# Kernel optimization log

Measured on AMD Instinct MI355X. Metric: run time of the kernel, lower is better.

The kernel has to match this reference:

```python
import jax, jax.numpy as jnp
import numpy as np

B, N, C, H, P, DP = 2, 1024, 768, 12, 4, 64
CH = C // H
SCALE = CH ** -0.5
EPS = 1e-5


def setup_inputs() -> dict:
    key = jax.random.key(0)
    ks = jax.random.split(key, 24)
    w = lambda k, s: jax.random.normal(k, s, jnp.float32) * 0.02
    inp = {
        'single': jax.random.normal(ks[0], (B, N, C), jnp.float32),
        'pair': jax.random.normal(ks[1], (B, N, N, DP), jnp.float32),
        'rot': jax.random.normal(ks[2], (B, N, 3, 3), jnp.float32),
        'trans': jax.random.normal(ks[3], (B, N, 3), jnp.float32),
        'mask': jnp.ones((B, N), dtype=bool),
        'Wq': w(ks[4], (C, C)), 'bq': jnp.zeros((C,), jnp.float32),
        'Wk': w(ks[5], (C, C)), 'bk': jnp.zeros((C,), jnp.float32),
        'Wv': w(ks[6], (C, C)), 'bv': jnp.zeros((C,), jnp.float32),
        'Wpb': w(ks[7], (DP, H)), 'bpb': jnp.zeros((H,), jnp.float32),
        'Wqp': w(ks[8], (C, H * P * 3)), 'bqp': jnp.zeros((H * P * 3,), jnp.float32),
        'Wkp': w(ks[9], (C, H * P * 3)), 'bkp': jnp.zeros((H * P * 3,), jnp.float32),
        'Wvp': w(ks[10], (C, H * P * 3)), 'bvp': jnp.zeros((H * P * 3,), jnp.float32),
        'Wo': w(ks[11], (C, C)), 'bo': jnp.zeros((C,), jnp.float32),
        'Wpo': w(ks[12], (H * P * 3, C)), 'bpo': jnp.zeros((C,), jnp.float32),
        'gamma': jnp.ones((C,), jnp.float32), 'beta': jnp.zeros((C,), jnp.float32),
    }
    return inp


def _ipa(single, pair, rot, trans, mask,
         Wq, bq, Wk, bk, Wv, bv, Wpb, bpb,
         Wqp, bqp, Wkp, bkp, Wvp, bvp,
         Wo, bo, Wpo, bpo, gamma, beta):
    # scalar q/k/v: [B,N,H,CH]
    q = (single @ Wq + bq).reshape(B, N, H, CH)
    k = (single @ Wk + bk).reshape(B, N, H, CH)
    v = (single @ Wv + bv).reshape(B, N, H, CH)
    # pair bias: [B,H,N,N]
    pair_bias = jnp.transpose(pair @ Wpb + bpb, (0, 3, 1, 2))
    # point q/k/v in local frames: [B,N,H,P,3]
    q_pts = (single @ Wqp + bqp).reshape(B, N, H, P, 3)
    k_pts = (single @ Wkp + bkp).reshape(B, N, H, P, 3)
    v_pts = (single @ Wvp + bvp).reshape(B, N, H, P, 3)
    # rotate into global frame and translate
    t = trans[:, :, None, None, :]  # [B,N,1,1,3]
    rt = lambda pts: jnp.einsum('bnhpd,bnde->bnhpe', pts, rot) + t
    q_pts, k_pts, v_pts = rt(q_pts), rt(k_pts), rt(v_pts)
    # squared norms: [B,H,N]
    q2 = jnp.transpose((q_pts ** 2).sum((3, 4)), (0, 2, 1))
    k2 = jnp.transpose((k_pts ** 2).sum((3, 4)), (0, 2, 1))
    # logits [B,H,M,N]
    scalar_logits = jnp.einsum('bmhc,bnhc->bhmn', q, k) * SCALE
    qk_pts = jnp.einsum('bmhpd,bnhpd->bhmn', q_pts, k_pts)
    point_logits = -0.5 * (q2[:, :, :, None] + k2[:, :, None, :] - 2.0 * qk_pts) * SCALE
    logits = scalar_logits + point_logits + pair_bias
    mask2d = mask[:, None, :, None] & mask[:, None, None, :]
    logits = jnp.where(mask2d, logits, -1e9)
    attn = jax.nn.softmax(logits, axis=-1)
    # dual output aggregation
    out_scalar = jnp.einsum('bhmn,bnhc->bmhc', attn, v).reshape(B, N, C)
    out_points = jnp.einsum('bhmn,bnhpd->bmhpd', attn, v_pts).reshape(B, N, H * P * 3)
    out = (out_scalar @ Wo + bo) + (out_points @ Wpo + bpo)
    x = single + out
    mu = x.mean(-1, keepdims=True)
    var = ((x - mu) ** 2).mean(-1, keepdims=True)
    return (x - mu) * jax.lax.rsqrt(var + EPS) * gamma + beta


def reference(single, pair, rot, trans, mask,
              Wq, bq, Wk, bk, Wv, bv, Wpb, bpb,
              Wqp, bqp, Wkp, bkp, Wvp, bvp,
              Wo, bo, Wpo, bpo, gamma, beta):
    return _ipa(single, pair, rot, trans, mask,
                Wq, bq, Wk, bk, Wv, bv, Wpb, bpb,
                Wqp, bqp, Wkp, bkp, Wvp, bvp,
                Wo, bo, Wpo, bpo, gamma, beta)
```

## Files before the change

### kernel.cpp

```cpp
#include <hip/hip_runtime.h>
#include <hip/hip_bf16.h>

#define B_ 2
#define N_ 1024
#define C_ 768
#define H_ 12
#define CH_ 64
#define P_ 4
#define DP_ 64
#define HP3 144
#define SCALE_ 0.125f
#define FATS 2816
#define K2_ 960
#define NCHUNK 2

typedef __attribute__((ext_vector_type(8))) short short8;
typedef __attribute__((ext_vector_type(4))) float f32x4;

__device__ __forceinline__ short f2bf(float f) {
  __hip_bfloat16 h = __float2bfloat16(f);
  return *reinterpret_cast<short*>(&h);
}
__device__ __forceinline__ float bf2f(unsigned short u) {
  __hip_bfloat16 h;
  *reinterpret_cast<unsigned short*>(&h) = u;
  return __bfloat162float(h);
}

__global__ __launch_bounds__(256) void prep_misc(
    const float* __restrict__ single, unsigned short* __restrict__ Sbf,
    const float* __restrict__ Wq, const float* __restrict__ Wk,
    const float* __restrict__ Wv, const float* __restrict__ Wqp,
    const float* __restrict__ Wkp, const float* __restrict__ Wvp,
    unsigned short* __restrict__ WT1,
    const float* __restrict__ Wo, const float* __restrict__ Wpo,
    unsigned short* __restrict__ W2T,
    const float* __restrict__ bq, const float* __restrict__ bk,
    const float* __restrict__ bv, const float* __restrict__ bqp,
    const float* __restrict__ bkp, const float* __restrict__ bvp,
    const float* __restrict__ bo, const float* __restrict__ bpo,
    float* __restrict__ bcat1, float* __restrict__ bias2)
{
  __shared__ float t[16][17];
  const int tid = threadIdx.x;
  const int bid = blockIdx.x;
  if (bid < 8448) {
    const int bx = bid % 48, by = bid / 48;
    const int rr = tid >> 4, cc = tid & 15;
    const int kk0 = bx * 16, nn0 = by * 16;
    const float* W = nullptr; int ncol0 = 0, Nw = 768;
    if (nn0 < 2304) {
      int s = nn0 / 768;
      W = (s == 0) ? Wq : (s == 1 ? Wk : Wv);
      ncol0 = nn0 - s * 768; Nw = 768;
    } else if (nn0 < 2736) {
      int s = (nn0 - 2304) / 144;
      W = (s == 0) ? Wqp : (s == 1 ? Wkp : Wvp);
      ncol0 = nn0 - 2304 - s * 144; Nw = 144;
    }
    t[rr][cc] = W ? W[(size_t)(kk0 + rr) * Nw + ncol0 + cc] : 0.f;
    __syncthreads();
    WT1[(size_t)(nn0 + rr) * 768 + kk0 + cc] = (unsigned short)f2bf(t[cc][rr]);
  } else if (bid < 11328) {
    const int lb = bid - 8448;
    const int bx = lb % 60, by = lb / 60;
    const int rr = tid >> 4, cc = tid & 15;
    const int kk0 = bx * 16, nn0 = by * 16;
    const int k2 = kk0 + rr, h = k2 / 80, c80 = k2 - h * 80;
    float v = 0.f;
    if (c80 < 64)      v = Wo[(size_t)(h * 64 + c80) * 768 + nn0 + cc];
    else if (c80 < 76) v = Wpo[(size_t)(h * 12 + c80 - 64) * 768 + nn0 + cc];
    t[rr][cc] = v;
    __syncthreads();
    W2T[(size_t)(nn0 + rr) * 960 + kk0 + cc] = (unsigned short)f2bf(t[cc][rr]);
  } else if (bid < 11339) {
    const int idx = (bid - 11328) * 256 + tid;
    if (idx < 2816) {
      float v = 0.f;
      if (idx < 2304) { int s = idx / 768; const float* p = s == 0 ? bq : (s == 1 ? bk : bv); v = p[idx - s * 768]; }
      else if (idx < 2736) { int s = (idx - 2304) / 144; const float* p = s == 0 ? bqp : (s == 1 ? bkp : bvp); v = p[idx - 2304 - s * 144]; }
      bcat1[idx] = v;
    }
    if (idx < 768) bias2[idx] = bo[idx] + bpo[idx];
  } else {
    const int idx = (bid - 11339) * 256 + tid;
    const float4 v = reinterpret_cast<const float4*>(single)[idx];
    union { unsigned short u[4]; uint2 v2; } o;
    o.u[0] = (unsigned short)f2bf(v.x); o.u[1] = (unsigned short)f2bf(v.y);
    o.u[2] = (unsigned short)f2bf(v.z); o.u[3] = (unsigned short)f2bf(v.w);
    reinterpret_cast<uint2*>(Sbf)[idx] = o.v2;
  }
}

template<int BM>
__global__ __launch_bounds__(256) void gemm_bf16(
    const unsigned short* __restrict__ A, int lda,
    const unsigned short* __restrict__ BT, int ldb, int K,
    float* __restrict__ out, int ldo, const float* __restrict__ bias)
{
  constexpr int BN = 64;
  constexpr int MI = BM / 32;
  constexpr int NJ = 2;
  __shared__ __align__(16) unsigned short As[BM][40];
  __shared__ __align__(16) unsigned short Bs[BN][40];
  const int tid = threadIdx.x;
  const int w = tid >> 6, l = tid & 63, r16 = l & 15, g = l >> 4;
  const int wr = w >> 1, wc = w & 1;
  const int bm = blockIdx.y * BM, bn = blockIdx.x * BN;
  f32x4 acc[MI][NJ];
  #pragma unroll
  for (int mi = 0; mi < MI; ++mi)
    #pragma unroll
    for (int nj = 0; nj < NJ; ++nj) {
      acc[mi][nj][0] = 0.f; acc[mi][nj][1] = 0.f;
      acc[mi][nj][2] = 0.f; acc[mi][nj][3] = 0.f;
    }
  for (int k0 = 0; k0 < K; k0 += 32) {
    #pragma unroll
    for (int i = 0; i < BM / 64; ++i) {
      const int idx = tid + 256 * i;
      const int row = idx >> 2, q4 = idx & 3;
      *(uint4*)&As[row][q4 * 8] =
          *(const uint4*)&A[(size_t)(bm + row) * lda + k0 + q4 * 8];
    }
    {
      const int row = tid >> 2, q4 = tid & 3;
      if (row < BN)
        *(uint4*)&Bs[row][q4 * 8] =
            *(const uint4*)&BT[(size_t)(bn + row) * ldb + k0 + q4 * 8];
    }
    __syncthreads();
    short8 af[MI], bfr[NJ];
    #pragma unroll
    for (int mi = 0; mi < MI; ++mi)
      af[mi] = *(const short8*)&As[wr * (BM / 2) + mi * 16 + r16][g * 8];
    #pragma unroll
    for (int nj = 0; nj < NJ; ++nj)
      bfr[nj] = *(const short8*)&Bs[wc * 32 + nj * 16 + r16][g * 8];
    #pragma unroll
    for (int mi = 0; mi < MI; ++mi)
      #pragma unroll
      for (int nj = 0; nj < NJ; ++nj)
        acc[mi][nj] = __builtin_amdgcn_mfma_f32_16x16x32_bf16(
            af[mi], bfr[nj], acc[mi][nj], 0, 0, 0);
    __syncthreads();
  }
  #pragma unroll
  for (int mi = 0; mi < MI; ++mi)
    #pragma unroll
    for (int nj = 0; nj < NJ; ++nj) {
      const int n = bn + wc * 32 + nj * 16 + r16;
      const float bn_ = bias[n];
      #pragma unroll
      for (int reg = 0; reg < 4; ++reg) {
        const int m = bm + wr * (BM / 2) + mi * 16 + g * 4 + reg;
        out[(size_t)m * ldo + n] = acc[mi][nj][reg] + bn_;
      }
    }
}

__global__ __launch_bounds__(128) void prep_qkv(
    const float* __restrict__ fat, const float* __restrict__ rot,
    const float* __restrict__ trans,
    __hip_bfloat16* __restrict__ Qaug, __hip_bfloat16* __restrict__ Kaug,
    __hip_bfloat16* __restrict__ Vtg)
{
  __shared__ float pts[3][12];
  __shared__ float s2[2];
  const int tid = threadIdx.x;
  const int bn = blockIdx.x, h = blockIdx.y;
  const int b = bn >> 10, n = bn & 1023;
  const int bh = b * H_ + h;
  const float* row = fat + (size_t)bn * FATS;
  if (tid < 36) {
    const int set = tid / 12, j = tid - set * 12;
    const int p = j / 3, e = j - p * 3;
    const float* src = row + 2304 + set * 144 + h * 12 + p * 3;
    const float d0 = src[0], d1 = src[1], d2 = src[2];
    const float* rr = rot + (size_t)bn * 9;
    pts[set][j] = d0 * rr[e] + d1 * rr[3 + e] + d2 * rr[6 + e]
                  + trans[(size_t)bn * 3 + e];
  }
  __syncthreads();
  if (tid < 2) {
    float s = 0.f;
    #pragma unroll
    for (int j = 0; j < 12; ++j) s += pts[tid][j] * pts[tid][j];
    s2[tid] = s;
  }
  __syncthreads();
  const int c = tid;
  if (c < 96) {
    float qv, kv;
    if (c < 64) {
      qv = SCALE_ * row[h * CH_ + c];
      kv = row[768 + h * CH_ + c];
    } else if (c < 76) {
      qv = SCALE_ * pts[0][c - 64];
      kv = pts[1][c - 64];
    } else if (c == 76) {
      qv = -0.5f * SCALE_ * s2[0];
      kv = 1.0f;
    } else if (c == 77) {
      qv = -0.5f * SCALE_;
      kv = s2[1];
    } else { qv = 0.f; kv = 0.f; }
    const size_t orow = ((size_t)bh << 10) + n;
    Qaug[orow * 96 + c] = __float2bfloat16(qv);
    Kaug[orow * 96 + c] = __float2bfloat16(kv);
  }
  if (c < 80) {
    float vv = 0.f;
    if (c < 64) vv = row[1536 + h * CH_ + c];
    else if (c < 76) vv = pts[2][c - 64];
    Vtg[(((size_t)bh * 80 + c) << 10) + n] = __float2bfloat16(vv);
  }
}

__global__ __launch_bounds__(256) void pair_bias_mfma(
    const float* __restrict__ pair, const float* __restrict__ Wpb,
    const float* __restrict__ bpb, unsigned short* __restrict__ pb)
{
  __shared__ __align__(16) short WpbT[16][72];
  __shared__ float bpb_s[16];
  __shared__ unsigned short PBs[256][18];
  const int tid = threadIdx.x;
  const int w = tid >> 6, l = tid & 63, r16 = l & 15, g = l >> 4;
  const size_t F0 = (size_t)blockIdx.x * 256;
  const int b = (int)(F0 >> 20);
  const int mn0 = (int)(F0 & 1048575);
  #pragma unroll
  for (int i = 0; i < 4; ++i) {
    int idx = tid + 256 * i;
    int hh = idx & 15, d = idx >> 4;
    WpbT[hh][d] = f2bf(hh < 12 ? Wpb[d * 12 + hh] : 0.f);
  }
  if (tid < 16) bpb_s[tid] = (tid < 12) ? bpb[tid] : 0.f;
  __syncthreads();
  #pragma unroll
  for (int rg = 0; rg < 4; ++rg) {
    const size_t Fr = F0 + w * 64 + rg * 16 + r16;
    const float* src = pair + Fr * 64;
    const float bias = bpb_s[r16];
    f32x4 acc;
    acc[0] = bias; acc[1] = bias; acc[2] = bias; acc[3] = bias;
    #pragma unroll
    for (int ks = 0; ks < 2; ++ks) {
      const f32x4 a0 = __builtin_nontemporal_load(
          reinterpret_cast<const f32x4*>(src + ks * 32 + g * 8));
      const f32x4 a1 = __builtin_nontemporal_load(
          reinterpret_cast<const f32x4*>(src + ks * 32 + g * 8 + 4));
      short8 ap;
      ap[0] = f2bf(a0[0]); ap[1] = f2bf(a0[1]); ap[2] = f2bf(a0[2]); ap[3] = f2bf(a0[3]);
      ap[4] = f2bf(a1[0]); ap[5] = f2bf(a1[1]); ap[6] = f2bf(a1[2]); ap[7] = f2bf(a1[3]);
      const short8 bw = *(const short8*)&WpbT[r16][ks * 32 + g * 8];
      acc = __builtin_amdgcn_mfma_f32_16x16x32_bf16(ap, bw, acc, 0, 0, 0);
    }
    #pragma unroll
    for (int reg = 0; reg < 4; ++reg)
      PBs[w * 64 + rg * 16 + 4 * g + reg][r16] = (unsigned short)f2bf(acc[reg]);
  }
  __syncthreads();
  #pragma unroll
  for (int hh = 0; hh < 12; ++hh)
    pb[((size_t)(b * 12 + hh) << 20) + mn0 + tid] = PBs[tid][hh];
}

__global__ __launch_bounds__(256) void flash_attn_part(
    const __hip_bfloat16* __restrict__ Qaug, const __hip_bfloat16* __restrict__ Kaug,
    const __hip_bfloat16* __restrict__ Vtg, const unsigned short* __restrict__ pb,
    unsigned short* __restrict__ pacc, float* __restrict__ pml)
{
  __shared__ __align__(16) short Ks[64][104];
  __shared__ __align__(16) short Vt[80][72];
  __shared__ __align__(16) short Ps[64][72];
  const int tid = threadIdx.x;
  const int w = tid >> 6, l = tid & 63, r16 = l & 15, g = l >> 4;
  const int m0 = blockIdx.x * 64;
  const int h = blockIdx.y;
  const int b = blockIdx.z >> 1, chunk = blockIdx.z & 1;
  const int bh = b * H_ + h;
  const uint4* Kg = (const uint4*)Kaug;
  const uint4* Vg = (const uint4*)Vtg;
  short8 qreg[3];
  {
    const unsigned short* qrow =
        (const unsigned short*)Qaug + (size_t)((bh << 10) + m0 + w * 16 + r16) * 96;
    #pragma unroll
    for (int ks = 0; ks < 3; ++ks)
      qreg[ks] = *(const short8*)&qrow[ks * 32 + g * 8];
  }
  float rm[4], rl[4];
  f32x4 acc[5];
  #pragma unroll
  for (int r = 0; r < 4; ++r) { rm[r] = -1e30f; rl[r] = 0.f; }
  #pragma unroll
  for (int ct = 0; ct < 5; ++ct) {
    acc[ct][0] = 0.f; acc[ct][1] = 0.f; acc[ct][2] = 0.f; acc[ct][3] = 0.f;
  }
  for (int t = chunk * (16 / NCHUNK); t < (chunk + 1) * (16 / NCHUNK); ++t) {
    const int n0 = t * 64;
    {
      const int r = tid >> 2, q = tid & 3;
      #pragma unroll
      for (int i = 0; i < 3; ++i) {
        const int c8 = q + 4 * i;
        *(uint4*)&Ks[r][c8 * 8] = Kg[(size_t)((bh << 10) + n0 + r) * 12 + c8];
      }
      #pragma unroll
      for (int i = 0; i < 3; ++i) {
        const int ch = tid + 256 * i;
        if (ch < 640) {
          const int cc = ch >> 3, j8 = ch & 7;
          *(uint4*)&Vt[cc][j8 * 8] = Vg[(size_t)(bh * 80 + cc) * 128 + (n0 >> 3) + j8];
        }
      }
    }
    f32x4 s[4];
    {
      const unsigned short* pbrow = pb + ((size_t)bh << 20) + n0 + r16;
      #pragma unroll
      for (int j = 0; j < 4; ++j)
        #pragma unroll
        for (int reg = 0; reg < 4; ++reg)
          s[j][reg] = bf2f(pbrow[((size_t)(m0 + w * 16 + 4 * g + reg) << 10) + 16 * j]);
    }
    __syncthreads();
    #pragma unroll
    for (int ks = 0; ks < 3; ++ks) {
      #pragma unroll
      for (int j = 0; j < 4; ++j) {
        const short8 bK = *(const short8*)&Ks[16 * j + r16][ks * 32 + g * 8];
        s[j] = __builtin_amdgcn_mfma_f32_16x16x32_bf16(qreg[ks], bK, s[j], 0, 0, 0);
      }
    }
    #pragma unroll
    for (int reg = 0; reg < 4; ++reg) {
      float tm = fmaxf(fmaxf(s[0][reg], s[1][reg]), fmaxf(s[2][reg], s[3][reg]));
      tm = fmaxf(tm, __shfl_xor(tm, 1));
      tm = fmaxf(tm, __shfl_xor(tm, 2));
      tm = fmaxf(tm, __shfl_xor(tm, 4));
      tm = fmaxf(tm, __shfl_xor(tm, 8));
      const float nm = fmaxf(rm[reg], tm);
      const float fac = __expf(rm[reg] - nm);
      rm[reg] = nm;
      float ps = 0.f;
      #pragma unroll
      for (int j = 0; j < 4; ++j) {
        const float p = __expf(s[j][reg] - nm);
        s[j][reg] = p;
        ps += p;
      }
      ps += __shfl_xor(ps, 1);
      ps += __shfl_xor(ps, 2);
      ps += __shfl_xor(ps, 4);
      ps += __shfl_xor(ps, 8);
      rl[reg] = rl[reg] * fac + ps;
      #pragma unroll
      for (int ct = 0; ct < 5; ++ct) acc[ct][reg] *= fac;
    }
    #pragma unroll
    for (int j = 0; j < 4; ++j)
      #pragma unroll
      for (int reg = 0; reg < 4; ++reg)
        Ps[w * 16 + 4 * g + reg][16 * j + r16] = f2bf(s[j][reg]);
    __syncthreads();
    #pragma unroll
    for (int ks = 0; ks < 2; ++ks) {
      const short8 aP = *(const short8*)&Ps[w * 16 + r16][ks * 32 + g * 8];
      #pragma unroll
      for (int ct = 0; ct < 5; ++ct) {
        const short8 bV = *(const short8*)&Vt[ct * 16 + r16][ks * 32 + g * 8];
        acc[ct] = __builtin_amdgcn_mfma_f32_16x16x32_bf16(aP, bV, acc[ct], 0, 0, 0);
      }
    }
    __syncthreads();
  }
  #pragma unroll
  for (int reg = 0; reg < 4; ++reg) {
    const int row = (bh << 10) + m0 + w * 16 + 4 * g + reg;
    const size_t base = ((size_t)chunk * 24576 + row) * 80;
    #pragma unroll
    for (int ct = 0; ct < 5; ++ct)
      pacc[base + ct * 16 + r16] = (unsigned short)f2bf(acc[ct][reg]);
    if (r16 == 0) {
      pml[((size_t)chunk * 24576 + row) * 2]     = rm[reg];
      pml[((size_t)chunk * 24576 + row) * 2 + 1] = rl[reg];
    }
  }
}

__global__ __launch_bounds__(256) void gemm2_fused(
    const unsigned short* __restrict__ pacc, const float* __restrict__ pml,
    const unsigned short* __restrict__ BT, float* __restrict__ out,
    const float* __restrict__ bias)
{
  __shared__ __align__(16) unsigned short As[64][40];
  __shared__ __align__(16) unsigned short Bs[64][40];
  __shared__ float w0_s[64][12], w1_s[64][12];
  const int tid = threadIdx.x;
  const int w = tid >> 6, l = tid & 63, r16 = l & 15, g = l >> 4;
  const int wr = w >> 1, wc = w & 1;
  const int bm = blockIdx.y * 64, bn = blockIdx.x * 64;
  for (int i = tid; i < 64 * 12; i += 256) {
    const int row = i / 12, h = i - row * 12;
    const int grow = bm + row;
    const int b = grow >> 10, m = grow & 1023;
    const size_t pr = ((size_t)(b * 12 + h) << 10) + m;
    const float m0 = pml[pr * 2],              l0 = pml[pr * 2 + 1];
    const float m1 = pml[(24576 + pr) * 2],    l1 = pml[(24576 + pr) * 2 + 1];
    const float M = fmaxf(m0, m1);
    const float e0 = __expf(m0 - M), e1 = __expf(m1 - M);
    const float inv = 1.f / (l0 * e0 + l1 * e1);
    w0_s[row][h] = e0 * inv;
    w1_s[row][h] = e1 * inv;
  }
  f32x4 acc[2][2];
  #pragma unroll
  for (int mi = 0; mi < 2; ++mi)
    #pragma unroll
    for (int nj = 0; nj < 2; ++nj) {
      acc[mi][nj][0] = 0.f; acc[mi][nj][1] = 0.f;
      acc[mi][nj][2] = 0.f; acc[mi][nj][3] = 0.f;
    }
  __syncthreads();
  for (int k0 = 0; k0 < 960; k0 += 32) {
    {
      const int row = tid >> 2, q4 = tid & 3;
      const int k2 = k0 + q4 * 8;
      const int h = k2 / 80, c = k2 - h * 80;
      const int grow = bm + row;
      const int b = grow >> 10, m = grow & 1023;
      const size_t pr = ((size_t)(b * 12 + h) << 10) + m;
      const short8 p0 = *(const short8*)&pacc[pr * 80 + c];
      const short8 p1 = *(const short8*)&pacc[(size_t)24576 * 80 + pr * 80 + c];
      const float w0 = w0_s[row][h], w1 = w1_s[row][h];
      short8 av;
      #pragma unroll
      for (int j = 0; j < 8; ++j)
        av[j] = f2bf(bf2f((unsigned short)p0[j]) * w0 +
                     bf2f((unsigned short)p1[j]) * w1);
      *(short8*)&As[row][q4 * 8] = av;
      *(uint4*)&Bs[row][q4 * 8] =
          *(const uint4*)&BT[(size_t)(bn + row) * 960 + k0 + q4 * 8];
    }
    __syncthreads();
    short8 af[2], bfr[2];
    #pragma unroll
    for (int mi = 0; mi < 2; ++mi)
      af[mi] = *(const short8*)&As[wr * 32 + mi * 16 + r16][g * 8];
    #pragma unroll
    for (int nj = 0; nj < 2; ++nj)
      bfr[nj] = *(const short8*)&Bs[wc * 32 + nj * 16 + r16][g * 8];
    #pragma unroll
    for (int mi = 0; mi < 2; ++mi)
      #pragma unroll
      for (int nj = 0; nj < 2; ++nj)
        acc[mi][nj] = __builtin_amdgcn_mfma_f32_16x16x32_bf16(
            af[mi], bfr[nj], acc[mi][nj], 0, 0, 0);
    __syncthreads();
  }
  #pragma unroll
  for (int mi = 0; mi < 2; ++mi)
    #pragma unroll
    for (int nj = 0; nj < 2; ++nj) {
      const int n = bn + wc * 32 + nj * 16 + r16;
      const float bn_ = bias[n];
      #pragma unroll
      for (int reg = 0; reg < 4; ++reg) {
        const int m = bm + wr * 32 + mi * 16 + g * 4 + reg;
        out[(size_t)m * 768 + n] = acc[mi][nj][reg] + bn_;
      }
    }
}

__global__ __launch_bounds__(256) void ln_kernel(
    const float* __restrict__ single, const float* __restrict__ tmp,
    const float* __restrict__ gamma, const float* __restrict__ beta,
    float* __restrict__ out)
{
  __shared__ float x_s[C_];
  __shared__ float rs1[4], rs2[4];
  const int row = blockIdx.x, tid = threadIdx.x;
  const int lane = tid & 63, wave = tid >> 6;
  const size_t base = (size_t)row * C_;
  float s1 = 0.f, s2 = 0.f;
  for (int i = tid; i < C_; i += 256) {
    float x = single[base + i] + tmp[base + i];
    x_s[i] = x;
    s1 += x;
    s2 += x * x;
  }
  #pragma unroll
  for (int off = 32; off > 0; off >>= 1) {
    s1 += __shfl_xor(s1, off);
    s2 += __shfl_xor(s2, off);
  }
  if (!lane) { rs1[wave] = s1; rs2[wave] = s2; }
  __syncthreads();
  const float S1 = rs1[0] + rs1[1] + rs1[2] + rs1[3];
  const float S2 = rs2[0] + rs2[1] + rs2[2] + rs2[3];
  const float mu = S1 * (1.f / C_);
  const float var = S2 * (1.f / C_) - mu * mu;
  const float inv = rsqrtf(var + 1e-5f);
  for (int i = tid; i < C_; i += 256)
    out[base + i] = (x_s[i] - mu) * inv * gamma[i] + beta[i];
}

extern "C" void kernel_launch(void* const* d_in, const int* in_sizes, int n_in,
                              void* d_out, int out_size, void* d_ws, size_t ws_size,
                              hipStream_t stream) {
  const float* single = (const float*)d_in[0];
  const float* pair   = (const float*)d_in[1];
  const float* rot    = (const float*)d_in[2];
  const float* trans  = (const float*)d_in[3];
  const float* Wq  = (const float*)d_in[5];
  const float* bq  = (const float*)d_in[6];
  const float* Wk  = (const float*)d_in[7];
  const float* bk  = (const float*)d_in[8];
  const float* Wv  = (const float*)d_in[9];
  const float* bv  = (const float*)d_in[10];
  const float* Wpb = (const float*)d_in[11];
  const float* bpb = (const float*)d_in[12];
  const float* Wqp = (const float*)d_in[13];
  const float* bqp = (const float*)d_in[14];
  const float* Wkp = (const float*)d_in[15];
  const float* bkp = (const float*)d_in[16];
  const float* Wvp = (const float*)d_in[17];
  const float* bvp = (const float*)d_in[18];
  const float* Wo  = (const float*)d_in[19];
  const float* bo  = (const float*)d_in[20];
  const float* Wpo = (const float*)d_in[21];
  const float* bpo = (const float*)d_in[22];
  const float* gamma = (const float*)d_in[23];
  const float* beta  = (const float*)d_in[24];

  float* ws = (float*)d_ws;
  float* fat  = ws;
  float* tmpb = ws + 5767168;
  unsigned short* pbb  = (unsigned short*)(ws + 7340032);
  __hip_bfloat16* Qaug = (__hip_bfloat16*)(ws + 19922944);
  __hip_bfloat16* Kaug = (__hip_bfloat16*)(ws + 21102592);
  __hip_bfloat16* Vtg  = (__hip_bfloat16*)(ws + 22282240);
  unsigned short* Sbf  = (unsigned short*)(ws + 23265280);
  unsigned short* WT1  = (unsigned short*)(ws + 24051712);
  unsigned short* W2T  = (unsigned short*)(ws + 25133056);
  float* bcat1 = ws + 25501696;
  float* bias2 = ws + 25504512;
  unsigned short* pacc = (unsigned short*)(ws + 26488576);
  float* pml  = ws + 30420736;

  const dim3 blk(256);
  prep_misc<<<12875, blk, 0, stream>>>(single, Sbf, Wq, Wk, Wv, Wqp, Wkp, Wvp,
                                       WT1, Wo, Wpo, W2T, bq, bk, bv, bqp, bkp,
                                       bvp, bo, bpo, bcat1, bias2);
  gemm_bf16<128><<<dim3(44, 16), blk, 0, stream>>>(Sbf, 768, WT1, 768, 768,
                                                   fat, FATS, bcat1);
  prep_qkv<<<dim3(2048, 12), dim3(128), 0, stream>>>(fat, rot, trans, Qaug, Kaug, Vtg);
  pair_bias_mfma<<<8192, blk, 0, stream>>>(pair, Wpb, bpb, pbb);
  flash_attn_part<<<dim3(16, 12, 2 * NCHUNK), blk, 0, stream>>>(
      Qaug, Kaug, Vtg, pbb, pacc, pml);
  gemm2_fused<<<dim3(12, 32), blk, 0, stream>>>(pacc, pml, W2T, tmpb, bias2);
  ln_kernel<<<2048, blk, 0, stream>>>(single, tmpb, gamma, beta, (float*)d_out);
}
```

Before: 251.3 us.

## Merge projection GEMM with pair-bias kernel and restructure prep_qkv per row

Combines the first projection GEMM and the pair-bias MFMA kernel into one launch that picks its role from the block index, so the small 704-block GEMM runs alongside the bandwidth-bound pair-bias blocks. prep_qkv now uses one 256-thread block per token covering all heads instead of one 128-thread block per (token, head). It stages rot/trans in shared memory and transforms all points once. This removes a launch, fills the idle GPU during the small GEMM, and cuts redundant per-head work, at the cost of shared-memory use being the union of both branches.

```diff
diff --git a/kernel.cpp b/kernel.cpp
--- a/kernel.cpp
+++ b/kernel.cpp
@@ -92,178 +92,177 @@
   }
 }
 
-template<int BM>
-__global__ __launch_bounds__(256) void gemm_bf16(
-    const unsigned short* __restrict__ A, int lda,
-    const unsigned short* __restrict__ BT, int ldb, int K,
-    float* __restrict__ out, int ldo, const float* __restrict__ bias)
+__global__ __launch_bounds__(256) void gemm1_pair(
+    const unsigned short* __restrict__ A, const unsigned short* __restrict__ BT,
+    float* __restrict__ out, const float* __restrict__ bias,
+    const float* __restrict__ pair, const float* __restrict__ Wpb,
+    const float* __restrict__ bpb, unsigned short* __restrict__ pb)
 {
-  constexpr int BN = 64;
-  constexpr int MI = BM / 32;
-  constexpr int NJ = 2;
-  __shared__ __align__(16) unsigned short As[BM][40];
-  __shared__ __align__(16) unsigned short Bs[BN][40];
   const int tid = threadIdx.x;
   const int w = tid >> 6, l = tid & 63, r16 = l & 15, g = l >> 4;
-  const int wr = w >> 1, wc = w & 1;
-  const int bm = blockIdx.y * BM, bn = blockIdx.x * BN;
-  f32x4 acc[MI][NJ];
-  #pragma unroll
-  for (int mi = 0; mi < MI; ++mi)
-    #pragma unroll
-    for (int nj = 0; nj < NJ; ++nj) {
-      acc[mi][nj][0] = 0.f; acc[mi][nj][1] = 0.f;
-      acc[mi][nj][2] = 0.f; acc[mi][nj][3] = 0.f;
-    }
-  for (int k0 = 0; k0 < K; k0 += 32) {
-    #pragma unroll
-    for (int i = 0; i < BM / 64; ++i) {
-      const int idx = tid + 256 * i;
-      const int row = idx >> 2, q4 = idx & 3;
-      *(uint4*)&As[row][q4 * 8] =
-          *(const uint4*)&A[(size_t)(bm + row) * lda + k0 + q4 * 8];
-    }
-    {
-      const int row = tid >> 2, q4 = tid & 3;
-      if (row < BN)
-        *(uint4*)&Bs[row][q4 * 8] =
-            *(const uint4*)&BT[(size_t)(bn + row) * ldb + k0 + q4 * 8];
-    }
-    __syncthreads();
-    short8 af[MI], bfr[NJ];
-    #pragma unroll
-    for (int mi = 0; mi < MI; ++mi)
-      af[mi] = *(const short8*)&As[wr * (BM / 2) + mi * 16 + r16][g * 8];
-    #pragma unroll
-    for (int nj = 0; nj < NJ; ++nj)
-      bfr[nj] = *(const short8*)&Bs[wc * 32 + nj * 16 + r16][g * 8];
-    #pragma unroll
-    for (int mi = 0; mi < MI; ++mi)
-      #pragma unroll
-      for (int nj = 0; nj < NJ; ++nj)
-        acc[mi][nj] = __builtin_amdgcn_mfma_f32_16x16x32_bf16(
-            af[mi], bfr[nj], acc[mi][nj], 0, 0, 0);
-    __syncthreads();
-  }
-  #pragma unroll
-  for (int mi = 0; mi < MI; ++mi)
-    #pragma unroll
-    for (int nj = 0; nj < NJ; ++nj) {
-      const int n = bn + wc * 32 + nj * 16 + r16;
-      const float bn_ = bias[n];
-      #pragma unroll
-      for (int reg = 0; reg < 4; ++reg) {
-        const int m = bm + wr * (BM / 2) + mi * 16 + g * 4 + reg;
-        out[(size_t)m * ldo + n] = acc[mi][nj][reg] + bn_;
-      }
-    }
-}
-
-__global__ __launch_bounds__(128) void prep_qkv(
+  if (blockIdx.x < 704) {
+    __shared__ __align__(16) unsigned short As[128][40];
+    __shared__ __align__(16) unsigned short Bs[64][40];
+    const int wr = w >> 1, wc = w & 1;
+    const int bm = (blockIdx.x / 44) * 128, bn = (blockIdx.x % 44) * 64;
+    f32x4 acc[4][2];
+    #pragma unroll
+    for (int mi = 0; mi < 4; ++mi)
+      #pragma unroll
+      for (int nj = 0; nj < 2; ++nj) {
+        acc[mi][nj][0] = 0.f; acc[mi][nj][1] = 0.f;
+        acc[mi][nj][2] = 0.f; acc[mi][nj][3] = 0.f;
+      }
+    for (int k0 = 0; k0 < 768; k0 += 32) {
+      #pragma unroll
+      for (int i = 0; i < 2; ++i) {
+        const int idx = tid + 256 * i;
+        const int row = idx >> 2, q4 = idx & 3;
+        *(uint4*)&As[row][q4 * 8] =
+            *(const uint4*)&A[(size_t)(bm + row) * 768 + k0 + q4 * 8];
+      }
+      {
+        const int row = tid >> 2, q4 = tid & 3;
+        if (row < 64)
+          *(uint4*)&Bs[row][q4 * 8] =
+              *(const uint4*)&BT[(size_t)(bn + row) * 768 + k0 + q4 * 8];
+      }
+      __syncthreads();
+      short8 af[4], bfr[2];
+      #pragma unroll
+      for (int mi = 0; mi < 4; ++mi)
+        af[mi] = *(const short8*)&As[wr * 64 + mi * 16 + r16][g * 8];
+      #pragma unroll
+      for (int nj = 0; nj < 2; ++nj)
+        bfr[nj] = *(const short8*)&Bs[wc * 32 + nj * 16 + r16][g * 8];
+      #pragma unroll
+      for (int mi = 0; mi < 4; ++mi)
+        #pragma unroll
+        for (int nj = 0; nj < 2; ++nj)
+          acc[mi][nj] = __builtin_amdgcn_mfma_f32_16x16x32_bf16(
+              af[mi], bfr[nj], acc[mi][nj], 0, 0, 0);
+      __syncthreads();
+    }
+    #pragma unroll
+    for (int mi = 0; mi < 4; ++mi)
+      #pragma unroll
+      for (int nj = 0; nj < 2; ++nj) {
+        const int n = bn + wc * 32 + nj * 16 + r16;
+        const float bn_ = bias[n];
+        #pragma unroll
+        for (int reg = 0; reg < 4; ++reg) {
+          const int m = bm + wr * 64 + mi * 16 + g * 4 + reg;
+          out[(size_t)m * FATS + n] = acc[mi][nj][reg] + bn_;
+        }
+      }
+  } else {
+    __shared__ __align__(16) short WpbT[16][72];
+    __shared__ float bpb_s[16];
+    __shared__ unsigned short PBs[256][18];
+    const int bid = blockIdx.x - 704;
+    const size_t F0 = (size_t)bid * 256;
+    const int b = (int)(F0 >> 20);
+    const int mn0 = (int)(F0 & 1048575);
+    #pragma unroll
+    for (int i = 0; i < 4; ++i) {
+      int idx = tid + 256 * i;
+      int hh = idx & 15, d = idx >> 4;
+      WpbT[hh][d] = f2bf(hh < 12 ? Wpb[d * 12 + hh] : 0.f);
+    }
+    if (tid < 16) bpb_s[tid] = (tid < 12) ? bpb[tid] : 0.f;
+    __syncthreads();
+    #pragma unroll
+    for (int rg = 0; rg < 4; ++rg) {
+      const size_t Fr = F0 + w * 64 + rg * 16 + r16;
+      const float* src = pair + Fr * 64;
+      const float bias_ = bpb_s[r16];
+      f32x4 acc;
+      acc[0] = bias_; acc[1] = bias_; acc[2] = bias_; acc[3] = bias_;
+      #pragma unroll
+      for (int ks = 0; ks < 2; ++ks) {
+        const f32x4 a0 = __builtin_nontemporal_load(
+            reinterpret_cast<const f32x4*>(src + ks * 32 + g * 8));
+        const f32x4 a1 = __builtin_nontemporal_load(
+            reinterpret_cast<const f32x4*>(src + ks * 32 + g * 8 + 4));
+        short8 ap;
+        ap[0] = f2bf(a0[0]); ap[1] = f2bf(a0[1]); ap[2] = f2bf(a0[2]); ap[3] = f2bf(a0[3]);
+        ap[4] = f2bf(a1[0]); ap[5] = f2bf(a1[1]); ap[6] = f2bf(a1[2]); ap[7] = f2bf(a1[3]);
+        const short8 bw = *(const short8*)&WpbT[r16][ks * 32 + g * 8];
+        acc = __builtin_amdgcn_mfma_f32_16x16x32_bf16(ap, bw, acc, 0, 0, 0);
+      }
+      #pragma unroll
+      for (int reg = 0; reg < 4; ++reg)
+        PBs[w * 64 + rg * 16 + 4 * g + reg][r16] = (unsigned short)f2bf(acc[reg]);
+    }
+    __syncthreads();
+    #pragma unroll
+    for (int hh = 0; hh < 12; ++hh)
+      pb[((size_t)(b * 12 + hh) << 20) + mn0 + tid] = PBs[tid][hh];
+  }
+}
+
+__global__ __launch_bounds__(256) void prep_qkv(
     const float* __restrict__ fat, const float* __restrict__ rot,
     const float* __restrict__ trans,
     __hip_bfloat16* __restrict__ Qaug, __hip_bfloat16* __restrict__ Kaug,
     __hip_bfloat16* __restrict__ Vtg)
 {
-  __shared__ float pts[3][12];
-  __shared__ float s2[2];
+  __shared__ float pts_s[3][144];
+  __shared__ float s2_s[2][12];
+  __shared__ float rot_s[9];
+  __shared__ float trans_s[3];
   const int tid = threadIdx.x;
-  const int bn = blockIdx.x, h = blockIdx.y;
+  const int bn = blockIdx.x;
   const int b = bn >> 10, n = bn & 1023;
-  const int bh = b * H_ + h;
   const float* row = fat + (size_t)bn * FATS;
-  if (tid < 36) {
-    const int set = tid / 12, j = tid - set * 12;
-    const int p = j / 3, e = j - p * 3;
-    const float* src = row + 2304 + set * 144 + h * 12 + p * 3;
-    const float d0 = src[0], d1 = src[1], d2 = src[2];
-    const float* rr = rot + (size_t)bn * 9;
-    pts[set][j] = d0 * rr[e] + d1 * rr[3 + e] + d2 * rr[6 + e]
-                  + trans[(size_t)bn * 3 + e];
-  }
+  if (tid < 9) rot_s[tid] = rot[(size_t)bn * 9 + tid];
+  if (tid < 3) trans_s[tid] = trans[(size_t)bn * 3 + tid];
   __syncthreads();
-  if (tid < 2) {
+  for (int i = tid; i < 432; i += 256) {
+    const int set = i / 144, j = i - set * 144;
+    const int e = j % 3, base = j - e;
+    const float d0 = row[2304 + set * 144 + base];
+    const float d1 = row[2304 + set * 144 + base + 1];
+    const float d2 = row[2304 + set * 144 + base + 2];
+    pts_s[set][j] = d0 * rot_s[e] + d1 * rot_s[3 + e] + d2 * rot_s[6 + e]
+                    + trans_s[e];
+  }
+  __syncthreads();
+  if (tid < 24) {
+    const int set = tid / 12, h = tid - set * 12;
     float s = 0.f;
     #pragma unroll
-    for (int j = 0; j < 12; ++j) s += pts[tid][j] * pts[tid][j];
-    s2[tid] = s;
+    for (int j = 0; j < 12; ++j) s += pts_s[set][h * 12 + j] * pts_s[set][h * 12 + j];
+    s2_s[set][h] = s;
   }
   __syncthreads();
-  const int c = tid;
-  if (c < 96) {
+  for (int i = tid; i < 1152; i += 256) {
+    const int h = i / 96, c = i - h * 96;
     float qv, kv;
     if (c < 64) {
       qv = SCALE_ * row[h * CH_ + c];
       kv = row[768 + h * CH_ + c];
     } else if (c < 76) {
-      qv = SCALE_ * pts[0][c - 64];
-      kv = pts[1][c - 64];
+      qv = SCALE_ * pts_s[0][h * 12 + (c - 64)];
+      kv = pts_s[1][h * 12 + (c - 64)];
     } else if (c == 76) {
-      qv = -0.5f * SCALE_ * s2[0];
+      qv = -0.5f * SCALE_ * s2_s[0][h];
       kv = 1.0f;
     } else if (c == 77) {
       qv = -0.5f * SCALE_;
-      kv = s2[1];
+      kv = s2_s[1][h];
     } else { qv = 0.f; kv = 0.f; }
-    const size_t orow = ((size_t)bh << 10) + n;
+    const size_t orow = ((size_t)(b * H_ + h) << 10) + n;
     Qaug[orow * 96 + c] = __float2bfloat16(qv);
     Kaug[orow * 96 + c] = __float2bfloat16(kv);
   }
-  if (c < 80) {
+  for (int i = tid; i < 960; i += 256) {
+    const int h = i / 80, c = i - h * 80;
     float vv = 0.f;
     if (c < 64) vv = row[1536 + h * CH_ + c];
-    else if (c < 76) vv = pts[2][c - 64];
-    Vtg[(((size_t)bh * 80 + c) << 10) + n] = __float2bfloat16(vv);
-  }
-}
-
-__global__ __launch_bounds__(256) void pair_bias_mfma(
-    const float* __restrict__ pair, const float* __restrict__ Wpb,
-    const float* __restrict__ bpb, unsigned short* __restrict__ pb)
-{
-  __shared__ __align__(16) short WpbT[16][72];
-  __shared__ float bpb_s[16];
-  __shared__ unsigned short PBs[256][18];
-  const int tid = threadIdx.x;
-  const int w = tid >> 6, l = tid & 63, r16 = l & 15, g = l >> 4;
-  const size_t F0 = (size_t)blockIdx.x * 256;
-  const int b = (int)(F0 >> 20);
-  const int mn0 = (int)(F0 & 1048575);
-  #pragma unroll
-  for (int i = 0; i < 4; ++i) {
-    int idx = tid + 256 * i;
-    int hh = idx & 15, d = idx >> 4;
-    WpbT[hh][d] = f2bf(hh < 12 ? Wpb[d * 12 + hh] : 0.f);
-  }
-  if (tid < 16) bpb_s[tid] = (tid < 12) ? bpb[tid] : 0.f;
-  __syncthreads();
-  #pragma unroll
-  for (int rg = 0; rg < 4; ++rg) {
-    const size_t Fr = F0 + w * 64 + rg * 16 + r16;
-    const float* src = pair + Fr * 64;
-    const float bias = bpb_s[r16];
-    f32x4 acc;
-    acc[0] = bias; acc[1] = bias; acc[2] = bias; acc[3] = bias;
-    #pragma unroll
-    for (int ks = 0; ks < 2; ++ks) {
-      const f32x4 a0 = __builtin_nontemporal_load(
-          reinterpret_cast<const f32x4*>(src + ks * 32 + g * 8));
-      const f32x4 a1 = __builtin_nontemporal_load(
-          reinterpret_cast<const f32x4*>(src + ks * 32 + g * 8 + 4));
-      short8 ap;
-      ap[0] = f2bf(a0[0]); ap[1] = f2bf(a0[1]); ap[2] = f2bf(a0[2]); ap[3] = f2bf(a0[3]);
-      ap[4] = f2bf(a1[0]); ap[5] = f2bf(a1[1]); ap[6] = f2bf(a1[2]); ap[7] = f2bf(a1[3]);
-      const short8 bw = *(const short8*)&WpbT[r16][ks * 32 + g * 8];
-      acc = __builtin_amdgcn_mfma_f32_16x16x32_bf16(ap, bw, acc, 0, 0, 0);
-    }
-    #pragma unroll
-    for (int reg = 0; reg < 4; ++reg)
-      PBs[w * 64 + rg * 16 + 4 * g + reg][r16] = (unsigned short)f2bf(acc[reg]);
-  }
-  __syncthreads();
-  #pragma unroll
-  for (int hh = 0; hh < 12; ++hh)
-    pb[((size_t)(b * 12 + hh) << 20) + mn0 + tid] = PBs[tid][hh];
+    else if (c < 76) vv = pts_s[2][h * 12 + (c - 64)];
+    Vtg[(((size_t)((b * H_ + h) * 80 + c)) << 10) + n] = __float2bfloat16(vv);
+  }
 }
 
 __global__ __launch_bounds__(256) void flash_attn_part(
@@ -554,10 +553,9 @@
   prep_misc<<<12875, blk, 0, stream>>>(single, Sbf, Wq, Wk, Wv, Wqp, Wkp, Wvp,
                                        WT1, Wo, Wpo, W2T, bq, bk, bv, bqp, bkp,
                                        bvp, bo, bpo, bcat1, bias2);
-  gemm_bf16<128><<<dim3(44, 16), blk, 0, stream>>>(Sbf, 768, WT1, 768, 768,
-                                                   fat, FATS, bcat1);
-  prep_qkv<<<dim3(2048, 12), dim3(128), 0, stream>>>(fat, rot, trans, Qaug, Kaug, Vtg);
-  pair_bias_mfma<<<8192, blk, 0, stream>>>(pair, Wpb, bpb, pbb);
+  gemm1_pair<<<704 + 8192, blk, 0, stream>>>(Sbf, WT1, fat, bcat1,
+                                             pair, Wpb, bpb, pbb);
+  prep_qkv<<<2048, blk, 0, stream>>>(fat, rot, trans, Qaug, Kaug, Vtg);
   flash_attn_part<<<dim3(16, 12, 2 * NCHUNK), blk, 0, stream>>>(
       Qaug, Kaug, Vtg, pbb, pacc, pml);
   gemm2_fused<<<dim3(12, 32), blk, 0, stream>>>(pacc, pml, W2T, tmpb, bias2);
```

New measurement: 240.7 us. -4.2%, faster.
